# Performance work log

Hardware: AMD Instinct MI355X
Metric: run time of the kernel (lower is better)

## Reference

```python
import jax, jax.numpy as jnp
import numpy as np

B, C, H, W = 4, 64, 64, 64
C8 = C // 8
OC = 64
K9 = 9


def setup_inputs() -> dict:
    key = jax.random.key(0)
    ks = jax.random.split(key, 8)
    x = jax.random.normal(ks[0], (B, C, H, W), dtype=jnp.float32)
    qw = jax.random.normal(ks[1], (C8, C), dtype=jnp.float32) * 0.05   # 1x1 conv weight
    qb = jax.random.normal(ks[2], (C8,), dtype=jnp.float32) * 0.05
    kw = jax.random.normal(ks[3], (C8, C), dtype=jnp.float32) * 0.05
    kb = jax.random.normal(ks[4], (C8,), dtype=jnp.float32) * 0.05
    gamma = jax.random.normal(ks[5], (1,), dtype=jnp.float32) * 0.1
    weight = jax.random.normal(ks[6], (OC, C, K9), dtype=jnp.float32) * 0.05
    bias = jnp.full((OC,), 0.1, dtype=jnp.float32)
    return {"x": x, "qw": qw, "qb": qb, "kw": kw, "kb": kb,
            "gamma": gamma, "weight": weight, "bias": bias}


def reference(x, qw, qb, kw, kb, gamma, weight, bias):
    b, c, h, w = x.shape
    hw = h * w
    # 1x1 convs -> (B, C8, HW)
    xf = x.reshape(b, c, hw)
    q = jnp.einsum('dc,bcn->bdn', qw, xf) + qb[None, :, None]
    k = jnp.einsum('dc,bcn->bdn', kw, xf) + kb[None, :, None]
    # energy[b,t,s] = <key[:,t], query[:,s]>  -> (B, HW, HW)
    energy = jnp.einsum('bdt,bds->bts', k, q)
    # top-9 source positions per target t; the torch boolean-mask gather
    # selects them in ascending index order, so sort the indices.
    _, idx = jax.lax.top_k(energy, K9)          # (B, HW, 9)
    idx = jnp.sort(idx, axis=-1)
    # gather x at selected positions: (B, HW, 9, C)
    x_t = xf.transpose(0, 2, 1)                 # (B, HW, C)
    gathered = jnp.take_along_axis(x_t[:, None, :, :], idx[:, :, :, None], axis=2)
    # out[b,o,j] = sum_{c,k} gathered[b,j,k,c] * weight[o,c,k] + bias[o]
    out = jnp.einsum('bjkc,ock->boj', gathered, weight) + bias[None, :, None]
    out = jax.nn.relu(out).reshape(b, c, h, w)
    return gamma[0] * out + x
```

## Files before the change

kernel.cpp:

```cpp
#include <hip/hip_runtime.h>
#include <math.h>

#define HW 4096
#define NB 4
#define LCAP 64

typedef unsigned short ushort_t;
typedef unsigned int uint_t;
typedef __attribute__((ext_vector_type(8))) short s8v;
typedef __attribute__((ext_vector_type(4))) float f32x4;

__device__ __forceinline__ ushort_t f2bf(float f) {
  uint_t u = __float_as_uint(f);
  u = (u + 0x7fffu + ((u >> 16) & 1u)) >> 16;
  return (ushort_t)u;
}
__device__ __forceinline__ float bf2f(ushort_t h) {
  uint_t u = ((uint_t)h) << 16;
  return __uint_as_float(u);
}

__device__ __forceinline__ float dot8(float4 klo, float4 khi, const float* qp) {
  float4 q0 = *(const float4*)qp;
  float4 q1 = *(const float4*)(qp + 4);
  float e = klo.x * q0.x;
  e = fmaf(klo.y, q0.y, e);
  e = fmaf(klo.z, q0.z, e);
  e = fmaf(klo.w, q0.w, e);
  e = fmaf(khi.x, q1.x, e);
  e = fmaf(khi.y, q1.y, e);
  e = fmaf(khi.z, q1.z, e);
  e = fmaf(khi.w, q1.w, e);
  return e;
}
__device__ __forceinline__ float dot8v(float4 klo, float4 khi, float4 q0, float4 q1) {
  float e = klo.x * q0.x;
  e = fmaf(klo.y, q0.y, e);
  e = fmaf(klo.z, q0.z, e);
  e = fmaf(klo.w, q0.w, e);
  e = fmaf(khi.x, q1.x, e);
  e = fmaf(khi.y, q1.y, e);
  e = fmaf(khi.z, q1.z, e);
  e = fmaf(khi.w, q1.w, e);
  return e;
}

__global__ __launch_bounds__(256) void qk_kernel(
    const float* __restrict__ x, const float* __restrict__ qw,
    const float* __restrict__ qb, const float* __restrict__ kw,
    const float* __restrict__ kb, const float* __restrict__ w,
    float* __restrict__ q_t, float* __restrict__ k_t, float* __restrict__ wt) {
  __shared__ float red[4][64][17];
  __shared__ float sqwT[512], skwT[512];
  int b = blockIdx.y;
  int sl = threadIdx.x & 63;
  int cg = threadIdx.x >> 6;
  int s = blockIdx.x * 64 + sl;

  {
    int bid = blockIdx.y * 64 + blockIdx.x;
    int gid = bid * 256 + threadIdx.x;
    if (gid < 64 * 64 * 9) {
      int o = gid / 576, rem = gid % 576, c = rem / 9, k = rem % 9;
      wt[(k * 64 + c) * 64 + o] = w[gid];
    }
  }

  for (int i = threadIdx.x; i < 512; i += 256) {
    int c = i >> 3, d = i & 7;
    sqwT[i] = qw[d * 64 + c];
    skwT[i] = kw[d * 64 + c];
  }
  __syncthreads();

  float qa[8], ka[8];
#pragma unroll
  for (int d = 0; d < 8; ++d) { qa[d] = 0.f; ka[d] = 0.f; }
  const float* xp = x + ((size_t)b * 64 + cg * 16) * HW + s;
#pragma unroll
  for (int c = 0; c < 16; ++c) {
    float xv = xp[(size_t)c * HW];
    int cc = cg * 16 + c;
    const float4 qw0 = *(const float4*)&sqwT[cc * 8];
    const float4 qw1 = *(const float4*)&sqwT[cc * 8 + 4];
    const float4 kw0 = *(const float4*)&skwT[cc * 8];
    const float4 kw1 = *(const float4*)&skwT[cc * 8 + 4];
    qa[0] = fmaf(qw0.x, xv, qa[0]); qa[1] = fmaf(qw0.y, xv, qa[1]);
    qa[2] = fmaf(qw0.z, xv, qa[2]); qa[3] = fmaf(qw0.w, xv, qa[3]);
    qa[4] = fmaf(qw1.x, xv, qa[4]); qa[5] = fmaf(qw1.y, xv, qa[5]);
    qa[6] = fmaf(qw1.z, xv, qa[6]); qa[7] = fmaf(qw1.w, xv, qa[7]);
    ka[0] = fmaf(kw0.x, xv, ka[0]); ka[1] = fmaf(kw0.y, xv, ka[1]);
    ka[2] = fmaf(kw0.z, xv, ka[2]); ka[3] = fmaf(kw0.w, xv, ka[3]);
    ka[4] = fmaf(kw1.x, xv, ka[4]); ka[5] = fmaf(kw1.y, xv, ka[5]);
    ka[6] = fmaf(kw1.z, xv, ka[6]); ka[7] = fmaf(kw1.w, xv, ka[7]);
  }
#pragma unroll
  for (int d = 0; d < 8; ++d) {
    red[cg][sl][d] = qa[d];
    red[cg][sl][8 + d] = ka[d];
  }
  __syncthreads();

#pragma unroll
  for (int r = 0; r < 4; ++r) {
    int f = r * 256 + threadIdx.x;
    int slf = f >> 4, dd = f & 15;
    float sum = red[0][slf][dd] + red[1][slf][dd] + red[2][slf][dd] + red[3][slf][dd];
    int ss_ = blockIdx.x * 64 + slf;
    if (dd < 8)
      q_t[((size_t)b * HW + ss_) * 8 + dd] = sum + qb[dd];
    else
      k_t[((size_t)b * HW + ss_) * 8 + (dd - 8)] = sum + kb[dd - 8];
  }
}

__global__ __launch_bounds__(256) void mid_kernel(
    const float* __restrict__ q_t, const float* __restrict__ k_t,
    const float* __restrict__ x, const float* __restrict__ wt,
    float* __restrict__ maxima, ushort_t* __restrict__ y) {
  __shared__ __align__(16) float smem[8192];
  int blk = blockIdx.x;
  int tid = threadIdx.x;

  if (blk < 1024) {
    float* qs = smem;
    int b = blk >> 8;
    int rem = blk & 255;
    int ch = rem >> 2;
    int tg = rem & 3;
    int lane = tid & 63;
    int w = tid >> 6;
    int t0 = tg * 1024 + w * 256 + 4 * lane;

    const float* kp = k_t + ((size_t)b * HW + t0) * 8;
    float4 ka0 = *(const float4*)(kp);      float4 ka1 = *(const float4*)(kp + 4);
    float4 kb0 = *(const float4*)(kp + 8);  float4 kb1 = *(const float4*)(kp + 12);
    float4 kc0 = *(const float4*)(kp + 16); float4 kc1 = *(const float4*)(kp + 20);
    float4 kd0 = *(const float4*)(kp + 24); float4 kd1 = *(const float4*)(kp + 28);

    if (tid < 128)
      *(float4*)&qs[tid * 4] =
          *(const float4*)&q_t[((size_t)b * HW + ch * 64) * 8 + tid * 4];
    __syncthreads();

    float m0 = -INFINITY, m1 = -INFINITY, m2 = -INFINITY, m3 = -INFINITY;
#pragma unroll 4
    for (int i = 0; i < 64; ++i) {
      float4 q0 = *(const float4*)&qs[i * 8];
      float4 q1 = *(const float4*)&qs[i * 8 + 4];
      m0 = fmaxf(m0, dot8v(ka0, ka1, q0, q1));
      m1 = fmaxf(m1, dot8v(kb0, kb1, q0, q1));
      m2 = fmaxf(m2, dot8v(kc0, kc1, q0, q1));
      m3 = fmaxf(m3, dot8v(kd0, kd1, q0, q1));
    }
    *(float4*)&maxima[((size_t)b * 64 + ch) * HW + t0] =
        make_float4(m0, m1, m2, m3);
  } else {
    ushort_t* Xh = (ushort_t*)smem;
    ushort_t* Xl = Xh + 64 * 72;
    ushort_t* Wb = Xl + 64 * 72;
    int task = blk - 1024;
    int b = task / 576;
    int rem = task % 576;
    int kk = rem / 64;
    int s0 = (rem % 64) * 64;

    {
      int sq = (tid & 7) | ((tid >> 3) & 8);
      int cq = ((tid >> 3) & 7) | ((tid >> 4) & 8);
      int q4 = sq * 4;

      const float* xp = x + ((size_t)b * 64 + cq * 4) * HW + s0 + q4;
      float4 r0 = *(const float4*)(xp);
      float4 r1 = *(const float4*)(xp + HW);
      float4 r2 = *(const float4*)(xp + 2 * HW);
      float4 r3 = *(const float4*)(xp + 3 * HW);
      float c0[4] = {r0.x, r0.y, r0.z, r0.w};
      float c1[4] = {r1.x, r1.y, r1.z, r1.w};
      float c2[4] = {r2.x, r2.y, r2.z, r2.w};
      float c3[4] = {r3.x, r3.y, r3.z, r3.w};
#pragma unroll
      for (int j = 0; j < 4; ++j) {
        ushort4 hh, ll;
        hh.x = f2bf(c0[j]); ll.x = f2bf(c0[j] - bf2f(hh.x));
        hh.y = f2bf(c1[j]); ll.y = f2bf(c1[j] - bf2f(hh.y));
        hh.z = f2bf(c2[j]); ll.z = f2bf(c2[j] - bf2f(hh.z));
        hh.w = f2bf(c3[j]); ll.w = f2bf(c3[j] - bf2f(hh.w));
        *(ushort4*)&Xh[(q4 + j) * 72 + cq * 4] = hh;
        *(ushort4*)&Xl[(q4 + j) * 72 + cq * 4] = ll;
      }

      const float* wp = wt + kk * 4096 + (cq * 4) * 64 + q4;
      float4 w0 = *(const float4*)(wp);
      float4 w1 = *(const float4*)(wp + 64);
      float4 w2 = *(const float4*)(wp + 128);
      float4 w3 = *(const float4*)(wp + 192);
      float d0[4] = {w0.x, w0.y, w0.z, w0.w};
      float d1[4] = {w1.x, w1.y, w1.z, w1.w};
      float d2[4] = {w2.x, w2.y, w2.z, w2.w};
      float d3[4] = {w3.x, w3.y, w3.z, w3.w};
#pragma unroll
      for (int j = 0; j < 4; ++j) {
        ushort4 hh;
        hh.x = f2bf(d0[j]); hh.y = f2bf(d1[j]);
        hh.z = f2bf(d2[j]); hh.w = f2bf(d3[j]);
        *(ushort4*)&Wb[(q4 + j) * 72 + cq * 4] = hh;
      }
    }
    __syncthreads();

    int w = tid >> 6;
    int lr = tid & 15;
    int lg = (tid & 63) >> 4;
    f32x4 acc0 = {0.f, 0.f, 0.f, 0.f};
    f32x4 acc1 = acc0, acc2 = acc0, acc3 = acc0;
#pragma unroll
    for (int ks = 0; ks < 2; ++ks) {
      int ko = ks * 32 + lg * 8;
      s8v ah = *(const s8v*)&Xh[(w * 16 + lr) * 72 + ko];
      s8v al = *(const s8v*)&Xl[(w * 16 + lr) * 72 + ko];
      s8v b0 = *(const s8v*)&Wb[(0 + lr) * 72 + ko];
      s8v b1 = *(const s8v*)&Wb[(16 + lr) * 72 + ko];
      s8v b2 = *(const s8v*)&Wb[(32 + lr) * 72 + ko];
      s8v b3 = *(const s8v*)&Wb[(48 + lr) * 72 + ko];
      acc0 = __builtin_amdgcn_mfma_f32_16x16x32_bf16(ah, b0, acc0, 0, 0, 0);
      acc1 = __builtin_amdgcn_mfma_f32_16x16x32_bf16(ah, b1, acc1, 0, 0, 0);
      acc2 = __builtin_amdgcn_mfma_f32_16x16x32_bf16(ah, b2, acc2, 0, 0, 0);
      acc3 = __builtin_amdgcn_mfma_f32_16x16x32_bf16(ah, b3, acc3, 0, 0, 0);
      acc0 = __builtin_amdgcn_mfma_f32_16x16x32_bf16(al, b0, acc0, 0, 0, 0);
      acc1 = __builtin_amdgcn_mfma_f32_16x16x32_bf16(al, b1, acc1, 0, 0, 0);
      acc2 = __builtin_amdgcn_mfma_f32_16x16x32_bf16(al, b2, acc2, 0, 0, 0);
      acc3 = __builtin_amdgcn_mfma_f32_16x16x32_bf16(al, b3, acc3, 0, 0, 0);
    }
    __syncthreads();

    ushort_t* Ly = (ushort_t*)smem;
#pragma unroll
    for (int r = 0; r < 4; ++r) {
      int s = w * 16 + lg * 4 + r;
      Ly[s * 72 + 0 + lr]  = f2bf(acc0[r]);
      Ly[s * 72 + 16 + lr] = f2bf(acc1[r]);
      Ly[s * 72 + 32 + lr] = f2bf(acc2[r]);
      Ly[s * 72 + 48 + lr] = f2bf(acc3[r]);
    }
    __syncthreads();

    ushort_t* yp = y + ((size_t)(b * 9 + kk) * HW + s0) * 64;
#pragma unroll
    for (int it = 0; it < 2; ++it) {
      int f = it * 2048 + tid * 8;
      int s = f >> 6, o = f & 63;
      *(uint4*)&yp[(size_t)s * 64 + o] = *(const uint4*)&Ly[s * 72 + o];
    }
  }
}

__global__ __launch_bounds__(256) void topk_gather_kernel(
    const float* __restrict__ q_t, const float* __restrict__ k_t,
    const float* __restrict__ maxima, const ushort_t* __restrict__ y,
    const float* __restrict__ bias, const float* __restrict__ gamma,
    const float* __restrict__ x, float* __restrict__ out) {
  __shared__ float ldsM[64 * 17];
  __shared__ int sArr[4][LCAP];
  __shared__ float eArr[4][LCAP];
  __shared__ int idxl[4][9];
  __shared__ float T[64 * 17];
  int b = blockIdx.y;
  int lane = threadIdx.x & 63;
  int w = threadIdx.x >> 6;
  int t0 = blockIdx.x * 16;

#pragma unroll
  for (int it = 0; it < 4; ++it) {
    int idx = it * 256 + threadIdx.x;
    int ch = idx >> 4, dt = idx & 15;
    ldsM[ch * 17 + dt] = maxima[((size_t)b * 64 + ch) * HW + t0 + dt];
  }
  __syncthreads();

  float g = gamma[0];
  float bs = bias[lane];
  const ushort_t* yb = y + (size_t)b * 9 * HW * 64;

#pragma unroll 1
  for (int ti = 0; ti < 4; ++ti) {
    int jl = w * 4 + ti;
    int t = t0 + jl;

    const float* kp = k_t + ((size_t)b * HW + t) * 8;
    float4 klo = *(const float4*)kp;
    float4 khi = *(const float4*)(kp + 4);

    float val = ldsM[lane * 17 + jl];
    float keepmax = val;
    float tauv = -INFINITY;
#pragma unroll
    for (int r = 0; r < 9; ++r) {
      float wmax = val;
#pragma unroll
      for (int off = 1; off < 64; off <<= 1)
        wmax = fmaxf(wmax, __shfl_xor(wmax, off, 64));
      tauv = wmax;
      unsigned long long m = __ballot(val == wmax);
      if (lane == (int)__builtin_ctzll(m)) val = -INFINITY;
    }

    unsigned long long mask = __ballot(keepmax >= tauv);
    int cnt = 0;
    while (mask) {
      int p = (int)__builtin_ctzll(mask);
      mask &= mask - 1;
      int s = p * 64 + lane;
      float e = dot8(klo, khi, q_t + ((size_t)b * HW + s) * 8);
      bool keep = e >= tauv;
      unsigned long long km = __ballot(keep);
      if (keep) {
        int pos = cnt + (int)__popcll(km & ((1ull << lane) - 1ull));
        if (pos < LCAP) { sArr[w][pos] = s; eArr[w][pos] = e; }
      }
      cnt += (int)__popcll(km);
    }
    if (cnt > LCAP) cnt = LCAP;

    float em = -INFINITY; int sm = 0x7fffffff;
    if (lane < cnt) { em = eArr[w][lane]; sm = sArr[w][lane]; }
    int rank = 0;
    for (int i = 0; i < cnt; ++i) {
      float ei = eArr[w][i];
      int si = sArr[w][i];
      rank += ((ei > em) || (ei == em && si < sm)) ? 1 : 0;
    }
    bool sel = (lane < cnt) && (rank < 9);
    unsigned long long smask = __ballot(sel);
    int pos = (int)__popcll(smask & ((1ull << lane) - 1ull));
    if (sel) idxl[w][pos] = sm;

    float acc = bs;
#pragma unroll
    for (int k = 0; k < 9; ++k) {
      int p9 = idxl[w][k];
      acc += bf2f(yb[((size_t)k * HW + p9) * 64 + lane]);
    }
    T[lane * 17 + jl] = g * fmaxf(acc, 0.f);
  }
  __syncthreads();

  for (int f = threadIdx.x; f < 1024; f += 256) {
    int o = f >> 4, jl = f & 15;
    size_t gi = ((size_t)b * 64 + o) * HW + t0 + jl;
    out[gi] = T[o * 17 + jl] + x[gi];
  }
}

extern "C" void kernel_launch(void* const* d_in, const int* in_sizes, int n_in,
                              void* d_out, int out_size, void* d_ws, size_t ws_size,
                              hipStream_t stream) {
  const float* x = (const float*)d_in[0];
  const float* qw = (const float*)d_in[1];
  const float* qb = (const float*)d_in[2];
  const float* kw = (const float*)d_in[3];
  const float* kb = (const float*)d_in[4];
  const float* gamma = (const float*)d_in[5];
  const float* weight = (const float*)d_in[6];
  const float* bias = (const float*)d_in[7];
  float* out = (float*)d_out;

  char* ws = (char*)d_ws;
  float* q_t = (float*)(ws);
  float* k_t = (float*)(ws + 524288);
  float* wt = (float*)(ws + 1048576);
  float* maxima = (float*)(ws + 1196032);
  ushort_t* y = (ushort_t*)(ws + 5390336);

  hipLaunchKernelGGL(qk_kernel, dim3(64, 4), dim3(256), 0, stream,
                     x, qw, qb, kw, kb, weight, q_t, k_t, wt);
  hipLaunchKernelGGL(mid_kernel, dim3(1024 + 2304), dim3(256), 0, stream,
                     q_t, k_t, x, wt, maxima, y);
  hipLaunchKernelGGL(topk_gather_kernel, dim3(256, 4), dim3(256), 0, stream,
                     q_t, k_t, maxima, y, bias, gamma, x, out);
}
```

Measured before the change: 122.6 us.

## Gather fp16 x rows and apply conv via MFMA after top-k instead of precomputing y

The mid kernel no longer precomputes a per-position, per-tap projection y (B×9×HW×64 bf16, built with split-hi/lo bf16 MFMAs). The qk kernel now also writes a transposed fp16 copy of x and an fp16 weight layout. The top-k kernel gathers the 9 selected x rows per target into LDS and runs 16x16x32 f16 MFMAs against the weights. This removes a large intermediate write and read and the extra GEMM blocks, at the cost of fp16 rounding of x and weights, plus a gather and an MFMA stage inside the top-k kernel.

```diff
diff --git a/kernel.cpp b/kernel.cpp
--- a/kernel.cpp
+++ b/kernel.cpp
@@ -7,17 +7,12 @@
 
 typedef unsigned short ushort_t;
 typedef unsigned int uint_t;
-typedef __attribute__((ext_vector_type(8))) short s8v;
+typedef __attribute__((ext_vector_type(8))) _Float16 f16x8;
 typedef __attribute__((ext_vector_type(4))) float f32x4;
 
-__device__ __forceinline__ ushort_t f2bf(float f) {
-  uint_t u = __float_as_uint(f);
-  u = (u + 0x7fffu + ((u >> 16) & 1u)) >> 16;
-  return (ushort_t)u;
-}
-__device__ __forceinline__ float bf2f(ushort_t h) {
-  uint_t u = ((uint_t)h) << 16;
-  return __uint_as_float(u);
+__device__ __forceinline__ ushort_t f2h(float f) {
+  _Float16 h = (_Float16)f;
+  return *(ushort_t*)&h;
 }
 
 __device__ __forceinline__ float dot8(float4 klo, float4 khi, const float* qp) {
@@ -49,7 +44,8 @@
     const float* __restrict__ x, const float* __restrict__ qw,
     const float* __restrict__ qb, const float* __restrict__ kw,
     const float* __restrict__ kb, const float* __restrict__ w,
-    float* __restrict__ q_t, float* __restrict__ k_t, float* __restrict__ wt) {
+    float* __restrict__ q_t, float* __restrict__ k_t,
+    ushort_t* __restrict__ xT, ushort_t* __restrict__ wt_h) {
   __shared__ float red[4][64][17];
   __shared__ float sqwT[512], skwT[512];
   int b = blockIdx.y;
@@ -62,7 +58,7 @@
     int gid = bid * 256 + threadIdx.x;
     if (gid < 64 * 64 * 9) {
       int o = gid / 576, rem = gid % 576, c = rem / 9, k = rem % 9;
-      wt[(k * 64 + c) * 64 + o] = w[gid];
+      wt_h[(k * 64 + o) * 64 + c] = f2h(w[gid]);
     }
   }
 
@@ -74,12 +70,14 @@
   __syncthreads();
 
   float qa[8], ka[8];
+  ushort_t h16[16];
 #pragma unroll
   for (int d = 0; d < 8; ++d) { qa[d] = 0.f; ka[d] = 0.f; }
   const float* xp = x + ((size_t)b * 64 + cg * 16) * HW + s;
 #pragma unroll
   for (int c = 0; c < 16; ++c) {
     float xv = xp[(size_t)c * HW];
+    h16[c] = f2h(xv);
     int cc = cg * 16 + c;
     const float4 qw0 = *(const float4*)&sqwT[cc * 8];
     const float4 qw1 = *(const float4*)&sqwT[cc * 8 + 4];
@@ -94,6 +92,11 @@
     ka[4] = fmaf(kw1.x, xv, ka[4]); ka[5] = fmaf(kw1.y, xv, ka[5]);
     ka[6] = fmaf(kw1.z, xv, ka[6]); ka[7] = fmaf(kw1.w, xv, ka[7]);
   }
+  {
+    ushort_t* xo = xT + (((size_t)b * HW + s) * 64 + cg * 16);
+    *(uint4*)&xo[0] = *(const uint4*)&h16[0];
+    *(uint4*)&xo[8] = *(const uint4*)&h16[8];
+  }
 #pragma unroll
   for (int d = 0; d < 8; ++d) {
     red[cg][sl][d] = qa[d];
@@ -116,155 +119,55 @@
 
 __global__ __launch_bounds__(256) void mid_kernel(
     const float* __restrict__ q_t, const float* __restrict__ k_t,
-    const float* __restrict__ x, const float* __restrict__ wt,
-    float* __restrict__ maxima, ushort_t* __restrict__ y) {
-  __shared__ __align__(16) float smem[8192];
+    float* __restrict__ maxima) {
+  __shared__ float qs[512];
   int blk = blockIdx.x;
   int tid = threadIdx.x;
-
-  if (blk < 1024) {
-    float* qs = smem;
-    int b = blk >> 8;
-    int rem = blk & 255;
-    int ch = rem >> 2;
-    int tg = rem & 3;
-    int lane = tid & 63;
-    int w = tid >> 6;
-    int t0 = tg * 1024 + w * 256 + 4 * lane;
-
-    const float* kp = k_t + ((size_t)b * HW + t0) * 8;
-    float4 ka0 = *(const float4*)(kp);      float4 ka1 = *(const float4*)(kp + 4);
-    float4 kb0 = *(const float4*)(kp + 8);  float4 kb1 = *(const float4*)(kp + 12);
-    float4 kc0 = *(const float4*)(kp + 16); float4 kc1 = *(const float4*)(kp + 20);
-    float4 kd0 = *(const float4*)(kp + 24); float4 kd1 = *(const float4*)(kp + 28);
-
-    if (tid < 128)
-      *(float4*)&qs[tid * 4] =
-          *(const float4*)&q_t[((size_t)b * HW + ch * 64) * 8 + tid * 4];
-    __syncthreads();
-
-    float m0 = -INFINITY, m1 = -INFINITY, m2 = -INFINITY, m3 = -INFINITY;
+  int b = blk >> 8;
+  int rem = blk & 255;
+  int ch = rem >> 2;
+  int tg = rem & 3;
+  int lane = tid & 63;
+  int w = tid >> 6;
+  int t0 = tg * 1024 + w * 256 + 4 * lane;
+
+  const float* kp = k_t + ((size_t)b * HW + t0) * 8;
+  float4 ka0 = *(const float4*)(kp);      float4 ka1 = *(const float4*)(kp + 4);
+  float4 kb0 = *(const float4*)(kp + 8);  float4 kb1 = *(const float4*)(kp + 12);
+  float4 kc0 = *(const float4*)(kp + 16); float4 kc1 = *(const float4*)(kp + 20);
+  float4 kd0 = *(const float4*)(kp + 24); float4 kd1 = *(const float4*)(kp + 28);
+
+  if (tid < 128)
+    *(float4*)&qs[tid * 4] =
+        *(const float4*)&q_t[((size_t)b * HW + ch * 64) * 8 + tid * 4];
+  __syncthreads();
+
+  float m0 = -INFINITY, m1 = -INFINITY, m2 = -INFINITY, m3 = -INFINITY;
 #pragma unroll 4
-    for (int i = 0; i < 64; ++i) {
-      float4 q0 = *(const float4*)&qs[i * 8];
-      float4 q1 = *(const float4*)&qs[i * 8 + 4];
-      m0 = fmaxf(m0, dot8v(ka0, ka1, q0, q1));
-      m1 = fmaxf(m1, dot8v(kb0, kb1, q0, q1));
-      m2 = fmaxf(m2, dot8v(kc0, kc1, q0, q1));
-      m3 = fmaxf(m3, dot8v(kd0, kd1, q0, q1));
-    }
-    *(float4*)&maxima[((size_t)b * 64 + ch) * HW + t0] =
-        make_float4(m0, m1, m2, m3);
-  } else {
-    ushort_t* Xh = (ushort_t*)smem;
-    ushort_t* Xl = Xh + 64 * 72;
-    ushort_t* Wb = Xl + 64 * 72;
-    int task = blk - 1024;
-    int b = task / 576;
-    int rem = task % 576;
-    int kk = rem / 64;
-    int s0 = (rem % 64) * 64;
-
-    {
-      int sq = (tid & 7) | ((tid >> 3) & 8);
-      int cq = ((tid >> 3) & 7) | ((tid >> 4) & 8);
-      int q4 = sq * 4;
-
-      const float* xp = x + ((size_t)b * 64 + cq * 4) * HW + s0 + q4;
-      float4 r0 = *(const float4*)(xp);
-      float4 r1 = *(const float4*)(xp + HW);
-      float4 r2 = *(const float4*)(xp + 2 * HW);
-      float4 r3 = *(const float4*)(xp + 3 * HW);
-      float c0[4] = {r0.x, r0.y, r0.z, r0.w};
-      float c1[4] = {r1.x, r1.y, r1.z, r1.w};
-      float c2[4] = {r2.x, r2.y, r2.z, r2.w};
-      float c3[4] = {r3.x, r3.y, r3.z, r3.w};
-#pragma unroll
-      for (int j = 0; j < 4; ++j) {
-        ushort4 hh, ll;
-        hh.x = f2bf(c0[j]); ll.x = f2bf(c0[j] - bf2f(hh.x));
-        hh.y = f2bf(c1[j]); ll.y = f2bf(c1[j] - bf2f(hh.y));
-        hh.z = f2bf(c2[j]); ll.z = f2bf(c2[j] - bf2f(hh.z));
-        hh.w = f2bf(c3[j]); ll.w = f2bf(c3[j] - bf2f(hh.w));
-        *(ushort4*)&Xh[(q4 + j) * 72 + cq * 4] = hh;
-        *(ushort4*)&Xl[(q4 + j) * 72 + cq * 4] = ll;
-      }
-
-      const float* wp = wt + kk * 4096 + (cq * 4) * 64 + q4;
-      float4 w0 = *(const float4*)(wp);
-      float4 w1 = *(const float4*)(wp + 64);
-      float4 w2 = *(const float4*)(wp + 128);
-      float4 w3 = *(const float4*)(wp + 192);
-      float d0[4] = {w0.x, w0.y, w0.z, w0.w};
-      float d1[4] = {w1.x, w1.y, w1.z, w1.w};
-      float d2[4] = {w2.x, w2.y, w2.z, w2.w};
-      float d3[4] = {w3.x, w3.y, w3.z, w3.w};
-#pragma unroll
-      for (int j = 0; j < 4; ++j) {
-        ushort4 hh;
-        hh.x = f2bf(d0[j]); hh.y = f2bf(d1[j]);
-        hh.z = f2bf(d2[j]); hh.w = f2bf(d3[j]);
-        *(ushort4*)&Wb[(q4 + j) * 72 + cq * 4] = hh;
-      }
-    }
-    __syncthreads();
-
-    int w = tid >> 6;
-    int lr = tid & 15;
-    int lg = (tid & 63) >> 4;
-    f32x4 acc0 = {0.f, 0.f, 0.f, 0.f};
-    f32x4 acc1 = acc0, acc2 = acc0, acc3 = acc0;
-#pragma unroll
-    for (int ks = 0; ks < 2; ++ks) {
-      int ko = ks * 32 + lg * 8;
-      s8v ah = *(const s8v*)&Xh[(w * 16 + lr) * 72 + ko];
-      s8v al = *(const s8v*)&Xl[(w * 16 + lr) * 72 + ko];
-      s8v b0 = *(const s8v*)&Wb[(0 + lr) * 72 + ko];
-      s8v b1 = *(const s8v*)&Wb[(16 + lr) * 72 + ko];
-      s8v b2 = *(const s8v*)&Wb[(32 + lr) * 72 + ko];
-      s8v b3 = *(const s8v*)&Wb[(48 + lr) * 72 + ko];
-      acc0 = __builtin_amdgcn_mfma_f32_16x16x32_bf16(ah, b0, acc0, 0, 0, 0);
-      acc1 = __builtin_amdgcn_mfma_f32_16x16x32_bf16(ah, b1, acc1, 0, 0, 0);
-      acc2 = __builtin_amdgcn_mfma_f32_16x16x32_bf16(ah, b2, acc2, 0, 0, 0);
-      acc3 = __builtin_amdgcn_mfma_f32_16x16x32_bf16(ah, b3, acc3, 0, 0, 0);
-      acc0 = __builtin_amdgcn_mfma_f32_16x16x32_bf16(al, b0, acc0, 0, 0, 0);
-      acc1 = __builtin_amdgcn_mfma_f32_16x16x32_bf16(al, b1, acc1, 0, 0, 0);
-      acc2 = __builtin_amdgcn_mfma_f32_16x16x32_bf16(al, b2, acc2, 0, 0, 0);
-      acc3 = __builtin_amdgcn_mfma_f32_16x16x32_bf16(al, b3, acc3, 0, 0, 0);
-    }
-    __syncthreads();
-
-    ushort_t* Ly = (ushort_t*)smem;
-#pragma unroll
-    for (int r = 0; r < 4; ++r) {
-      int s = w * 16 + lg * 4 + r;
-      Ly[s * 72 + 0 + lr]  = f2bf(acc0[r]);
-      Ly[s * 72 + 16 + lr] = f2bf(acc1[r]);
-      Ly[s * 72 + 32 + lr] = f2bf(acc2[r]);
-      Ly[s * 72 + 48 + lr] = f2bf(acc3[r]);
-    }
-    __syncthreads();
-
-    ushort_t* yp = y + ((size_t)(b * 9 + kk) * HW + s0) * 64;
-#pragma unroll
-    for (int it = 0; it < 2; ++it) {
-      int f = it * 2048 + tid * 8;
-      int s = f >> 6, o = f & 63;
-      *(uint4*)&yp[(size_t)s * 64 + o] = *(const uint4*)&Ly[s * 72 + o];
-    }
-  }
+  for (int i = 0; i < 64; ++i) {
+    float4 q0 = *(const float4*)&qs[i * 8];
+    float4 q1 = *(const float4*)&qs[i * 8 + 4];
+    m0 = fmaxf(m0, dot8v(ka0, ka1, q0, q1));
+    m1 = fmaxf(m1, dot8v(kb0, kb1, q0, q1));
+    m2 = fmaxf(m2, dot8v(kc0, kc1, q0, q1));
+    m3 = fmaxf(m3, dot8v(kd0, kd1, q0, q1));
+  }
+  *(float4*)&maxima[((size_t)b * 64 + ch) * HW + t0] =
+      make_float4(m0, m1, m2, m3);
 }
 
 __global__ __launch_bounds__(256) void topk_gather_kernel(
     const float* __restrict__ q_t, const float* __restrict__ k_t,
-    const float* __restrict__ maxima, const ushort_t* __restrict__ y,
-    const float* __restrict__ bias, const float* __restrict__ gamma,
-    const float* __restrict__ x, float* __restrict__ out) {
+    const float* __restrict__ maxima, const ushort_t* __restrict__ xT,
+    const ushort_t* __restrict__ wt_h, const float* __restrict__ bias,
+    const float* __restrict__ gamma, const float* __restrict__ x,
+    float* __restrict__ out) {
   __shared__ float ldsM[64 * 17];
   __shared__ int sArr[4][LCAP];
   __shared__ float eArr[4][LCAP];
-  __shared__ int idxl[4][9];
+  __shared__ int sIdx[16][9];
   __shared__ float T[64 * 17];
+  __shared__ __align__(16) ushort_t Gf[16 * 648];
   int b = blockIdx.y;
   int lane = threadIdx.x & 63;
   int w = threadIdx.x >> 6;
@@ -277,10 +180,6 @@
     ldsM[ch * 17 + dt] = maxima[((size_t)b * 64 + ch) * HW + t0 + dt];
   }
   __syncthreads();
-
-  float g = gamma[0];
-  float bs = bias[lane];
-  const ushort_t* yb = y + (size_t)b * 9 * HW * 64;
 
 #pragma unroll 1
   for (int ti = 0; ti < 4; ++ti) {
@@ -333,15 +232,43 @@
     bool sel = (lane < cnt) && (rank < 9);
     unsigned long long smask = __ballot(sel);
     int pos = (int)__popcll(smask & ((1ull << lane) - 1ull));
-    if (sel) idxl[w][pos] = sm;
-
-    float acc = bs;
+    if (sel) sIdx[jl][pos] = sm;
+  }
+  __syncthreads();
+
+  {
+    const ushort_t* xTb = xT + (size_t)b * HW * 64;
+#pragma unroll
+    for (int i = 0; i < 9; ++i) {
+      int pr = i * 256 + threadIdx.x;
+      int pair = pr >> 4;
+      int sub = pr & 15;
+      int t = pair / 9, k = pair - t * 9;
+      int p = sIdx[t][k];
+      *(uint2*)&Gf[t * 648 + k * 72 + sub * 4] =
+          *(const uint2*)&xTb[(size_t)p * 64 + sub * 4];
+    }
+  }
+  __syncthreads();
+
+  {
+    int lr = lane & 15, lg = lane >> 4;
+    f32x4 acc = {0.f, 0.f, 0.f, 0.f};
+    const ushort_t* wbase = wt_h + ((size_t)(w * 16 + lr)) * 64 + lg * 8;
 #pragma unroll
     for (int k = 0; k < 9; ++k) {
-      int p9 = idxl[w][k];
-      acc += bf2f(yb[((size_t)k * HW + p9) * 64 + lane]);
-    }
-    T[lane * 17 + jl] = g * fmaxf(acc, 0.f);
+      f16x8 a0 = *(const f16x8*)&Gf[lr * 648 + k * 72 + lg * 8];
+      f16x8 a1 = *(const f16x8*)&Gf[lr * 648 + k * 72 + 32 + lg * 8];
+      f16x8 b0 = *(const f16x8*)&wbase[(size_t)k * 4096];
+      f16x8 b1 = *(const f16x8*)&wbase[(size_t)k * 4096 + 32];
+      acc = __builtin_amdgcn_mfma_f32_16x16x32_f16(a0, b0, acc, 0, 0, 0);
+      acc = __builtin_amdgcn_mfma_f32_16x16x32_f16(a1, b1, acc, 0, 0, 0);
+    }
+    float g = gamma[0];
+    float bo = bias[w * 16 + lr];
+#pragma unroll
+    for (int r = 0; r < 4; ++r)
+      T[(w * 16 + lr) * 17 + lg * 4 + r] = g * fmaxf(acc[r] + bo, 0.f);
   }
   __syncthreads();
 
@@ -368,14 +295,14 @@
   char* ws = (char*)d_ws;
   float* q_t = (float*)(ws);
   float* k_t = (float*)(ws + 524288);
-  float* wt = (float*)(ws + 1048576);
-  float* maxima = (float*)(ws + 1196032);
-  ushort_t* y = (ushort_t*)(ws + 5390336);
+  float* maxima = (float*)(ws + 1048576);
+  ushort_t* xT = (ushort_t*)(ws + 5242880);
+  ushort_t* wt_h = (ushort_t*)(ws + 7340032);
 
   hipLaunchKernelGGL(qk_kernel, dim3(64, 4), dim3(256), 0, stream,
-                     x, qw, qb, kw, kb, weight, q_t, k_t, wt);
-  hipLaunchKernelGGL(mid_kernel, dim3(1024 + 2304), dim3(256), 0, stream,
-                     q_t, k_t, x, wt, maxima, y);
+                     x, qw, qb, kw, kb, weight, q_t, k_t, xT, wt_h);
+  hipLaunchKernelGGL(mid_kernel, dim3(1024), dim3(256), 0, stream,
+                     q_t, k_t, maxima);
   hipLaunchKernelGGL(topk_gather_kernel, dim3(256, 4), dim3(256), 0, stream,
-                     q_t, k_t, maxima, y, bias, gamma, x, out);
-}
+                     q_t, k_t, maxima, xT, wt_h, bias, gamma, x, out);
+}
```

Result: no change. 123.3 us (+0.5%).
